# Kernel optimization log

Hardware: AMD Instinct MI355X
Metric: run time of the kernel (lower is better)

The kernel has to match this reference:

```python
import jax, jax.numpy as jnp
import numpy as np

S, T, I = 4096, 64, 64          # spatial cells, timesteps, input features
EH, E, H = 128, 256, 512        # embedding hidden, embedding size, LSTM hidden
LG, O, F1, F2 = 32, 128, 256, 64


def setup_inputs() -> dict:
    key = jax.random.key(0)
    ks = jax.random.split(key, 24)
    w = lambda k, shape: jax.random.normal(k, shape, jnp.float32) * 0.05
    return {
        "inputData": jax.random.normal(ks[0], (S, T, I), jnp.float32),
        "lane": jax.random.uniform(ks[1], (1, 1), jnp.float32),
        # lane gate MLP
        "Wlg1": w(ks[2], (LG, 1)),  "blg1": w(ks[3], (LG,)),
        "Wlg2": w(ks[4], (1, LG)),  "blg2": w(ks[5], (1,)),
        # embedding MLP
        "We1": w(ks[6], (EH, I)),   "be1": w(ks[7], (EH,)),
        "We2": w(ks[8], (E, EH)),   "be2": w(ks[9], (E,)),
        # LSTMCell params (torch layout: [4H, in]/[4H, H], gate order i,f,g,o)
        "Wih": w(ks[10], (4 * H, E)), "bih": w(ks[11], (4 * H,)),
        "Whh": w(ks[12], (4 * H, H)), "bhh": w(ks[13], (4 * H,)),
        # output head
        "Wout": w(ks[14], (O, H)),  "bout": w(ks[15], (O,)),
        "Wf1": w(ks[16], (F1, O)),  "bf1": w(ks[17], (F1,)),
        "Wf2": w(ks[18], (F2, F1)), "bf2": w(ks[19], (F2,)),
        "Wf3": w(ks[20], (1, F2)),  "bf3": w(ks[21], (1,)),
    }


def _spatial_maxpool(h):
    # MaxPool1d(kernel=3, stride=1, padding=1) over the spatial axis (axis 0),
    # implicit -inf padding as in torch maxpool.
    hp = jnp.pad(h, ((1, 1), (0, 0)), constant_values=-jnp.inf)
    return jnp.maximum(jnp.maximum(hp[:-2], hp[1:-1]), hp[2:])


def reference(inputData, lane, Wlg1, blg1, Wlg2, blg2, We1, be1, We2, be2,
              Wih, bih, Whh, bhh, Wout, bout, Wf1, bf1, Wf2, bf2, Wf3, bf3):
    # lane gate -> scalar in (0,1)
    lg = jax.nn.relu(lane @ Wlg1.T + blg1)
    laneC = jax.nn.sigmoid(lg @ Wlg2.T + blg2)          # [1,1]
    x = inputData * laneC.reshape(1, 1, 1)              # [S,T,I]
    # embedding MLP
    x = jax.nn.relu(x @ We1.T + be1)
    x = jax.nn.relu(x @ We2.T + be2)                    # [S,T,E]
    xt = jnp.transpose(x, (1, 0, 2))                    # [T,S,E]

    def step(carry, x_t):
        h, c = carry
        gates = x_t @ Wih.T + bih + h @ Whh.T + bhh     # [S,4H]
        i, f, g, o = jnp.split(gates, 4, axis=-1)
        c = jax.nn.sigmoid(f) * c + jax.nn.sigmoid(i) * jnp.tanh(g)
        h = jax.nn.sigmoid(o) * jnp.tanh(c)
        h = _spatial_maxpool(h)
        return (h, c), None

    h0 = jnp.zeros((inputData.shape[0], H), jnp.float32)
    c0 = jnp.zeros((inputData.shape[0], H), jnp.float32)
    (h, c), _ = jax.lax.scan(step, (h0, c0), xt)

    out = h @ Wout.T + bout
    out = jax.nn.relu(out @ Wf1.T + bf1)
    out = jax.nn.relu(out @ Wf2.T + bf2)
    out = out @ Wf3.T + bf3                             # [S,1]
    out = out / laneC.reshape(-1, 1)
    return (out, h, c)
```

## Files before the change

### kernel.cpp

```cpp
#include <hip/hip_runtime.h>
#include <hip/hip_bf16.h>
#include <cstdint>
#include <cstddef>

using bf16 = __hip_bfloat16;

typedef __attribute__((ext_vector_type(8))) short s8vec;
typedef __attribute__((ext_vector_type(4))) float f4vec;

#define SD 4096
#define TD 64
#define ID 64
#define EHD 128
#define ED 256
#define HD 512
#define GD 2048
#define OD 128
#define F1D 256
#define F2D 64

__device__ __forceinline__ float sigmf(float x) { return 1.0f / (1.0f + __expf(-x)); }
__device__ __forceinline__ float tanh_fast(float x) { return 1.0f - 2.0f / (__expf(2.0f * x) + 1.0f); }

__device__ __forceinline__ void async16(const bf16* g, void* lds) {
    __builtin_amdgcn_global_load_lds(
        (const __attribute__((address_space(1))) void*)g,
        (__attribute__((address_space(3))) void*)lds, 16, 0, 0);
}

__global__ __launch_bounds__(256, 4)
void lstm_gemm(const bf16* __restrict__ xt,
               const bf16* __restrict__ h,
               const bf16* __restrict__ Wpack,
               const float* __restrict__ biasg,
               const float* __restrict__ c_in,
               float* __restrict__ c_out,
               bf16* __restrict__ h_pre)
{
    __shared__ __align__(16) bf16 As[128 * 64];
    __shared__ __align__(16) bf16 Bs[64 * 64];

    const int tid = threadIdx.x;
    const int lane = tid & 63;
    const int wm = tid >> 6;
    const int m0 = blockIdx.x * 128, n0 = blockIdx.y * 64;
    const int lm = lane & 15, lq = lane >> 4;

    f4vec acc[2][4];
#pragma unroll
    for (int i = 0; i < 2; ++i)
#pragma unroll
        for (int j = 0; j < 4; ++j) acc[i][j] = (f4vec){0.f, 0.f, 0.f, 0.f};

    for (int kc = 0; kc < ED + HD; kc += 64) {
        const bf16* Ab; int Alda, kk;
        if (kc < ED) { Ab = xt; Alda = ED; kk = kc; }
        else         { Ab = h;  Alda = HD; kk = kc - ED; }

#pragma unroll
        for (int it = 0; it < 4; ++it) {
            int flat = it * 256 + tid;
            int row = flat >> 3, colu = flat & 7;
            const bf16* ga = Ab + (size_t)(m0 + row) * Alda + kk + colu * 8;
            uint32_t off = (uint32_t)(it * 256 + (tid & ~63)) * 16u;
            async16(ga, (char*)As + off);
        }
#pragma unroll
        for (int it = 0; it < 2; ++it) {
            int flat = it * 256 + tid;
            int row = flat >> 3, colu = flat & 7;
            const bf16* gb = Wpack + (size_t)(n0 + row) * (ED + HD) + kc + colu * 8;
            uint32_t off = (uint32_t)(it * 256 + (tid & ~63)) * 16u;
            async16(gb, (char*)Bs + off);
        }
        __syncthreads();

#pragma unroll
        for (int ks = 0; ks < 64; ks += 32) {
            s8vec af[2], bfr[4];
#pragma unroll
            for (int mi = 0; mi < 2; ++mi)
                af[mi] = *(const s8vec*)(As + (wm * 32 + mi * 16 + lm) * 64 + ks + lq * 8);
#pragma unroll
            for (int ni = 0; ni < 4; ++ni)
                bfr[ni] = *(const s8vec*)(Bs + (ni * 16 + lm) * 64 + ks + lq * 8);
#pragma unroll
            for (int mi = 0; mi < 2; ++mi)
#pragma unroll
                for (int ni = 0; ni < 4; ++ni)
                    acc[mi][ni] = __builtin_amdgcn_mfma_f32_16x16x32_bf16(af[mi], bfr[ni], acc[mi][ni], 0, 0, 0);
        }
        __syncthreads();
    }

    const int j = (n0 >> 2) + lm;
    const float bi = biasg[n0 + lm];
    const float bff = biasg[n0 + 16 + lm];
    const float bg = biasg[n0 + 32 + lm];
    const float bo = biasg[n0 + 48 + lm];
#pragma unroll
    for (int mi = 0; mi < 2; ++mi) {
#pragma unroll
        for (int r = 0; r < 4; ++r) {
            const int row = m0 + wm * 32 + mi * 16 + lq * 4 + r;
            float gi = acc[mi][0][r] + bi;
            float gf = acc[mi][1][r] + bff;
            float gg = acc[mi][2][r] + bg;
            float go = acc[mi][3][r] + bo;
            float cn = sigmf(gf) * c_in[(size_t)row * HD + j] + sigmf(gi) * tanh_fast(gg);
            c_out[(size_t)row * HD + j] = cn;
            h_pre[(size_t)row * HD + j] = __float2bfloat16(sigmf(go) * tanh_fast(cn));
        }
    }
}

constexpr int MODE_BF16 = 0;
constexpr int MODE_SCATTER = 2;

template <int MODE>
__global__ __launch_bounds__(256, 2)
void gemm_kernel(const bf16* __restrict__ A1, int lda1,
                 const bf16* __restrict__ B, int ldb,
                 const float* __restrict__ bias,
                 const float* __restrict__ scale,
                 int relu, void* __restrict__ Cp, int ldc,
                 int K, int ncols)
{
    __shared__ __align__(16) bf16 As[128 * 64];
    __shared__ __align__(16) bf16 Bs[128 * 64];

    const int tid = threadIdx.x;
    const int lane = tid & 63;
    const int w = tid >> 6;
    const int wm = w & 1, wn = w >> 1;
    const int m0 = blockIdx.x * 128, n0 = blockIdx.y * 128;
    const int lm = lane & 15, lq = lane >> 4;

    f4vec acc[4][4];
#pragma unroll
    for (int i = 0; i < 4; ++i)
#pragma unroll
        for (int j = 0; j < 4; ++j) acc[i][j] = (f4vec){0.f, 0.f, 0.f, 0.f};

    for (int kc = 0; kc < K; kc += 64) {
#pragma unroll
        for (int it = 0; it < 4; ++it) {
            int flat = it * 256 + tid;
            int row = flat >> 3, colu = flat & 7;
            const bf16* ga = A1 + (size_t)(m0 + row) * lda1 + kc + colu * 8;
            const bf16* gb = B + (size_t)(n0 + row) * ldb + kc + colu * 8;
            uint32_t off = (uint32_t)(it * 256 + (tid & ~63)) * 16u;
            async16(ga, (char*)As + off);
            async16(gb, (char*)Bs + off);
        }
        __syncthreads();

#pragma unroll
        for (int ks = 0; ks < 64; ks += 32) {
            s8vec af[4], bfr[4];
#pragma unroll
            for (int mi = 0; mi < 4; ++mi)
                af[mi] = *(const s8vec*)(As + (wm * 64 + mi * 16 + lm) * 64 + ks + lq * 8);
#pragma unroll
            for (int ni = 0; ni < 4; ++ni)
                bfr[ni] = *(const s8vec*)(Bs + (wn * 64 + ni * 16 + lm) * 64 + ks + lq * 8);
#pragma unroll
            for (int mi = 0; mi < 4; ++mi)
#pragma unroll
                for (int ni = 0; ni < 4; ++ni)
                    acc[mi][ni] = __builtin_amdgcn_mfma_f32_16x16x32_bf16(af[mi], bfr[ni], acc[mi][ni], 0, 0, 0);
        }
        __syncthreads();
    }

    const float sc = scale ? scale[0] : 1.0f;
#pragma unroll
    for (int mi = 0; mi < 4; ++mi) {
#pragma unroll
        for (int ni = 0; ni < 4; ++ni) {
            const int gcol = n0 + wn * 64 + ni * 16 + lm;
            const float bv = bias[gcol];
#pragma unroll
            for (int r = 0; r < 4; ++r) {
                const int grow = m0 + wm * 64 + mi * 16 + lq * 4 + r;
                float v = acc[mi][ni][r] * sc + bv;
                if (relu) v = fmaxf(v, 0.f);
                if constexpr (MODE == MODE_BF16) {
                    if (gcol < ncols)
                        ((bf16*)Cp)[(size_t)grow * ldc + gcol] = __float2bfloat16(v);
                } else {
                    const int crow = (grow & 63) * SD + (grow >> 6);
                    ((bf16*)Cp)[(size_t)crow * ldc + gcol] = __float2bfloat16(v);
                }
            }
        }
    }
}

__global__ void prep_kernel(const float* __restrict__ Wih, const float* __restrict__ Whh,
                            const float* __restrict__ bih, const float* __restrict__ bhh,
                            const float* __restrict__ We1, const float* __restrict__ We2,
                            const float* __restrict__ Wout, const float* __restrict__ Wf1,
                            const float* __restrict__ Wf2, const float* __restrict__ bf2,
                            bf16* __restrict__ Wpack, float* __restrict__ biasg,
                            bf16* __restrict__ We1b, bf16* __restrict__ We2b,
                            bf16* __restrict__ Woutb, bf16* __restrict__ Wf1b,
                            bf16* __restrict__ Wf2p, float* __restrict__ bf2f)
{
    int idx = blockIdx.x * 256 + threadIdx.x;
    const int S0 = GD * (ED + HD);
    if (idx < S0) {
        int p = idx / (ED + HD), k = idx - p * (ED + HD);
        int gate = (p >> 4) & 3;
        int j = (p >> 6) * 16 + (p & 15);
        int orig = gate * HD + j;
        float v = (k < ED) ? Wih[(size_t)orig * ED + k] : Whh[(size_t)orig * HD + (k - ED)];
        Wpack[idx] = __float2bfloat16(v);
        return;
    }
    idx -= S0;
    if (idx < GD) {
        int p = idx;
        int gate = (p >> 4) & 3;
        int j = (p >> 6) * 16 + (p & 15);
        int orig = gate * HD + j;
        biasg[p] = bih[orig] + bhh[orig];
        return;
    }
    idx -= GD;
    if (idx < EHD * ID) { We1b[idx] = __float2bfloat16(We1[idx]); return; }
    idx -= EHD * ID;
    if (idx < ED * EHD) { We2b[idx] = __float2bfloat16(We2[idx]); return; }
    idx -= ED * EHD;
    if (idx < OD * HD) { Woutb[idx] = __float2bfloat16(Wout[idx]); return; }
    idx -= OD * HD;
    if (idx < F1D * OD) { Wf1b[idx] = __float2bfloat16(Wf1[idx]); return; }
    idx -= F1D * OD;
    if (idx < 128 * F1D) {
        int nrow = idx >> 8;
        Wf2p[idx] = (nrow < F2D) ? __float2bfloat16(Wf2[idx]) : __float2bfloat16(0.f);
        return;
    }
    idx -= 128 * F1D;
    if (idx < 128) { bf2f[idx] = (idx < F2D) ? bf2[idx] : 0.f; return; }
}

__global__ void cvt_input_kernel(const float* __restrict__ src, bf16* __restrict__ dst)
{
    int i = (blockIdx.x * 256 + threadIdx.x) * 8;
    float4 a = *(const float4*)(src + i);
    float4 b = *(const float4*)(src + i + 4);
    bf16 o[8] = { __float2bfloat16(a.x), __float2bfloat16(a.y),
                  __float2bfloat16(a.z), __float2bfloat16(a.w),
                  __float2bfloat16(b.x), __float2bfloat16(b.y),
                  __float2bfloat16(b.z), __float2bfloat16(b.w) };
    *(uint4*)(dst + i) = *(const uint4*)o;
}

__global__ void lane_kernel(const float* __restrict__ lane, const float* __restrict__ Wlg1,
                            const float* __restrict__ blg1, const float* __restrict__ Wlg2,
                            const float* __restrict__ blg2, float* __restrict__ laneC)
{
    if (threadIdx.x != 0) return;
    const float l = lane[0];
    float acc = blg2[0];
    for (int k = 0; k < 32; ++k)
        acc += fmaxf(l * Wlg1[k] + blg1[k], 0.f) * Wlg2[k];
    float v = 1.f / (1.f + __expf(-acc));
    laneC[0] = v;
    laneC[1] = 1.f / v;
}

__global__ void zero_kernel(float* __restrict__ c0, bf16* __restrict__ h)
{
    int idx = blockIdx.x * 256 + threadIdx.x;
    if (idx < SD * HD) { c0[idx] = 0.f; h[idx] = __float2bfloat16(0.f); }
}

__global__ void maxpool_kernel(const bf16* __restrict__ hp, bf16* __restrict__ hout)
{
    int base = (blockIdx.x * 256 + threadIdx.x) * 8;
    int s = base >> 9;
    const uint4 vm = *(const uint4*)(hp + base);
    const unsigned short* m = (const unsigned short*)&vm;
    uint4 vu, vd;
    const unsigned short* u = nullptr; const unsigned short* d = nullptr;
    if (s > 0)      { vu = *(const uint4*)(hp + base - HD); u = (const unsigned short*)&vu; }
    if (s < SD - 1) { vd = *(const uint4*)(hp + base + HD); d = (const unsigned short*)&vd; }
    unsigned short o[8];
#pragma unroll
    for (int e = 0; e < 8; ++e) {
        float v = __bfloat162float(__ushort_as_bfloat16(m[e]));
        if (u) v = fmaxf(v, __bfloat162float(__ushort_as_bfloat16(u[e])));
        if (d) v = fmaxf(v, __bfloat162float(__ushort_as_bfloat16(d[e])));
        o[e] = __bfloat16_as_ushort(__float2bfloat16(v));
    }
    *(uint4*)(hout + base) = *(const uint4*)o;
}

__global__ void f3_kernel(const bf16* __restrict__ xf2, const float* __restrict__ Wf3,
                          const float* __restrict__ bf3, const float* __restrict__ laneC,
                          float* __restrict__ out)
{
    int s = blockIdx.x * 256 + threadIdx.x;
    if (s >= SD) return;
    float acc = bf3[0];
#pragma unroll
    for (int k = 0; k < F2D; ++k)
        acc += __bfloat162float(xf2[(size_t)s * F2D + k]) * Wf3[k];
    out[s] = acc * laneC[1];
}

__global__ void finalize_kernel(const bf16* __restrict__ h, const float* __restrict__ c,
                                float* __restrict__ out)
{
    int idx = (blockIdx.x * 256 + threadIdx.x) * 4;
    if (idx >= SD * HD) return;
    uint2 hv4 = *(const uint2*)(h + idx);
    const unsigned short* hu = (const unsigned short*)&hv4;
    float4 hf = { __bfloat162float(__ushort_as_bfloat16(hu[0])),
                  __bfloat162float(__ushort_as_bfloat16(hu[1])),
                  __bfloat162float(__ushort_as_bfloat16(hu[2])),
                  __bfloat162float(__ushort_as_bfloat16(hu[3])) };
    *(float4*)(out + SD + idx) = hf;
    *(float4*)(out + SD + SD * HD + idx) = *(const float4*)(c + idx);
}

extern "C" void kernel_launch(void* const* d_in, const int* in_sizes, int n_in,
                              void* d_out, int out_size, void* d_ws, size_t ws_size,
                              hipStream_t stream)
{
    (void)in_sizes; (void)n_in; (void)out_size;
    const float* inputDataF = (const float*)d_in[0];
    const float* lane = (const float*)d_in[1];
    const float* Wlg1 = (const float*)d_in[2];
    const float* blg1 = (const float*)d_in[3];
    const float* Wlg2 = (const float*)d_in[4];
    const float* blg2 = (const float*)d_in[5];
    const float* We1 = (const float*)d_in[6];
    const float* be1 = (const float*)d_in[7];
    const float* We2 = (const float*)d_in[8];
    const float* be2 = (const float*)d_in[9];
    const float* Wih = (const float*)d_in[10];
    const float* bih = (const float*)d_in[11];
    const float* Whh = (const float*)d_in[12];
    const float* bhh = (const float*)d_in[13];
    const float* Wout = (const float*)d_in[14];
    const float* bout = (const float*)d_in[15];
    const float* Wf1 = (const float*)d_in[16];
    const float* bf1 = (const float*)d_in[17];
    const float* Wf2 = (const float*)d_in[18];
    const float* bf2 = (const float*)d_in[19];
    const float* Wf3 = (const float*)d_in[20];
    const float* bf3 = (const float*)d_in[21];
    float* out = (float*)d_out;

    char* wp = (char*)d_ws;
    auto carve = [&](size_t bytes) { char* p = wp; wp += (bytes + 255) & ~(size_t)255; return p; };

    bf16* inb   = (bf16*)carve((size_t)SD * TD * ID * 2);
    float* laneCbuf = (float*)carve(2 * sizeof(float));
    float* cbuf0 = (float*)carve((size_t)SD * HD * 4);
    float* cbuf1 = (float*)carve((size_t)SD * HD * 4);
    bf16* hbuf  = (bf16*)carve((size_t)SD * HD * 2);
    bf16* hpre  = (bf16*)carve((size_t)SD * HD * 2);
    bf16* Wpack = (bf16*)carve((size_t)GD * (ED + HD) * 2);
    float* biasg = (float*)carve(GD * 4);
    float* bf2f = (float*)carve(128 * 4);
    bf16* We1b  = (bf16*)carve((size_t)EHD * ID * 2);
    bf16* We2b  = (bf16*)carve((size_t)ED * EHD * 2);
    bf16* Woutb = (bf16*)carve((size_t)OD * HD * 2);
    bf16* Wf1b  = (bf16*)carve((size_t)F1D * OD * 2);
    bf16* Wf2p  = (bf16*)carve((size_t)128 * F1D * 2);
    bf16* out_o = (bf16*)carve((size_t)SD * OD * 2);
    bf16* xf1   = (bf16*)carve((size_t)SD * F1D * 2);
    bf16* xf2   = (bf16*)carve((size_t)SD * F2D * 2);

    const size_t SZ_X1 = (size_t)SD * TD * EHD * 2;
    const size_t SZ_X2 = (size_t)SD * TD * ED * 2;
    const size_t used = (size_t)(wp - (char*)d_ws);
    const size_t remain = (ws_size > used) ? (ws_size - used) : 0;
    const bool persist = remain >= (SZ_X1 + SZ_X2 + 4096);

    bf16* x1 = nullptr; bf16* x2 = nullptr;
    bf16* x1t = nullptr; bf16* x2t = nullptr;
    if (persist) {
        x1 = (bf16*)carve(SZ_X1);
        x2 = (bf16*)carve(SZ_X2);
    } else {
        x1t = (bf16*)carve((size_t)SD * EHD * 2);
        x2t = (bf16*)carve((size_t)SD * ED * 2);
    }

    const int PREP_N = GD * (ED + HD) + GD + EHD * ID + ED * EHD + OD * HD
                     + F1D * OD + 128 * F1D + 128;

    cvt_input_kernel<<<SD * TD * ID / (256 * 8), 256, 0, stream>>>(inputDataF, inb);
    prep_kernel<<<(PREP_N + 255) / 256, 256, 0, stream>>>(
        Wih, Whh, bih, bhh, We1, We2, Wout, Wf1, Wf2, bf2,
        Wpack, biasg, We1b, We2b, Woutb, Wf1b, Wf2p, bf2f);
    lane_kernel<<<1, 64, 0, stream>>>(lane, Wlg1, blg1, Wlg2, blg2, laneCbuf);
    zero_kernel<<<SD * HD / 256, 256, 0, stream>>>(cbuf0, hbuf);

    if (persist) {
        gemm_kernel<MODE_BF16><<<dim3(SD * TD / 128, 1), 256, 0, stream>>>(
            inb, ID, We1b, ID, be1, laneCbuf, 1, x1, EHD, ID, EHD);
        gemm_kernel<MODE_SCATTER><<<dim3(SD * TD / 128, ED / 128), 256, 0, stream>>>(
            x1, EHD, We2b, EHD, be2, nullptr, 1, x2, ED, EHD, ED);
    }

    for (int t = 0; t < TD; ++t) {
        const float* c_in = (t & 1) ? cbuf1 : cbuf0;
        float* c_out = (t & 1) ? cbuf0 : cbuf1;
        const bf16* xA;
        if (persist) {
            xA = x2 + (size_t)t * SD * ED;
        } else {
            gemm_kernel<MODE_BF16><<<dim3(SD / 128, 1), 256, 0, stream>>>(
                inb + (size_t)t * ID, TD * ID, We1b, ID, be1, laneCbuf, 1,
                x1t, EHD, ID, EHD);
            gemm_kernel<MODE_BF16><<<dim3(SD / 128, ED / 128), 256, 0, stream>>>(
                x1t, EHD, We2b, EHD, be2, nullptr, 1, x2t, ED, EHD, ED);
            xA = x2t;
        }
        lstm_gemm<<<dim3(SD / 128, GD / 64), 256, 0, stream>>>(
            xA, hbuf, Wpack, biasg, c_in, c_out, hpre);
        maxpool_kernel<<<SD * HD / (256 * 8), 256, 0, stream>>>(hpre, hbuf);
    }

    gemm_kernel<MODE_BF16><<<dim3(SD / 128, 1), 256, 0, stream>>>(
        hbuf, HD, Woutb, HD, bout, nullptr, 0, out_o, OD, HD, OD);
    gemm_kernel<MODE_BF16><<<dim3(SD / 128, F1D / 128), 256, 0, stream>>>(
        out_o, OD, Wf1b, OD, bf1, nullptr, 1, xf1, F1D, OD, F1D);
    gemm_kernel<MODE_BF16><<<dim3(SD / 128, 1), 256, 0, stream>>>(
        xf1, F1D, Wf2p, F1D, bf2f, nullptr, 1, xf2, F2D, F1D, F2D);
    f3_kernel<<<SD / 256, 256, 0, stream>>>(xf2, Wf3, bf3, laneCbuf, out);
    finalize_kernel<<<SD * HD / (256 * 4), 256, 0, stream>>>(hbuf, cbuf0, out);
}
```

Baseline: 2.466 ms.

## Run LSTM recurrence as persistent cooperative kernel with register-resident cell state

Replaces the 64 per-timestep lstm_gemm and maxpool launch pairs with one cooperative kernel that loops over timesteps and synchronises the grid between steps. The cell state stays in registers across steps, and the spatial maxpool is folded into the h-tile load. Tiles widen to 128x128 with a new weight/bias packing to match. The aim is to cut launch overhead and the round trips of c and h_pre through memory, at the cost of grid-wide barriers, a 256-block grid that must be co-resident, and synchronous (non-async) loads for the fused maxpool.

```diff
diff --git a/kernel.cpp b/kernel.cpp
--- a/kernel.cpp
+++ b/kernel.cpp
@@ -1,8 +1,10 @@
 #include <hip/hip_runtime.h>
 #include <hip/hip_bf16.h>
+#include <hip/hip_cooperative_groups.h>
 #include <cstdint>
 #include <cstddef>
 
+namespace cg = cooperative_groups;
 using bf16 = __hip_bfloat16;
 
 typedef __attribute__((ext_vector_type(8))) short s8vec;
@@ -28,64 +30,187 @@
         (__attribute__((address_space(3))) void*)lds, 16, 0, 0);
 }
 
-__global__ __launch_bounds__(256, 4)
-void lstm_gemm(const bf16* __restrict__ xt,
-               const bf16* __restrict__ h,
-               const bf16* __restrict__ Wpack,
-               const float* __restrict__ biasg,
-               const float* __restrict__ c_in,
-               float* __restrict__ c_out,
-               bf16* __restrict__ h_pre)
-{
+__device__ __forceinline__ float bfbits2f(unsigned short u) {
+    union { unsigned int i; float f; } v; v.i = (unsigned int)u << 16; return v.f;
+}
+
+__device__ __forceinline__ uint4 bfmax8(uint4 a, uint4 b) {
+    const unsigned short* pa = (const unsigned short*)&a;
+    const unsigned short* pb = (const unsigned short*)&b;
+    uint4 r; unsigned short* pr = (unsigned short*)&r;
+#pragma unroll
+    for (int e = 0; e < 8; ++e)
+        pr[e] = (bfbits2f(pa[e]) > bfbits2f(pb[e])) ? pa[e] : pb[e];
+    return r;
+}
+
+__global__ __launch_bounds__(256, 2)
+void lstm_persistent(const bf16* __restrict__ x2,
+                     bf16* __restrict__ hpA,
+                     bf16* __restrict__ hpB,
+                     const bf16* __restrict__ Wpack,
+                     const float* __restrict__ biasg,
+                     float* __restrict__ cbuf)
+{
+    cg::grid_group grid = cg::this_grid();
     __shared__ __align__(16) bf16 As[128 * 64];
-    __shared__ __align__(16) bf16 Bs[64 * 64];
+    __shared__ __align__(16) bf16 Bs[128 * 64];
 
     const int tid = threadIdx.x;
     const int lane = tid & 63;
-    const int wm = tid >> 6;
-    const int m0 = blockIdx.x * 128, n0 = blockIdx.y * 64;
+    const int w = tid >> 6;
+    const int wm = w & 1, wn = w >> 1;
+    const int m0 = blockIdx.x * 128, n0 = blockIdx.y * 128;
     const int lm = lane & 15, lq = lane >> 4;
-
-    f4vec acc[2][4];
-#pragma unroll
-    for (int i = 0; i < 2; ++i)
-#pragma unroll
-        for (int j = 0; j < 4; ++j) acc[i][j] = (f4vec){0.f, 0.f, 0.f, 0.f};
+    const int j = (n0 >> 2) + wn * 16 + lm;
+    const float bi = biasg[n0 + wn * 64 + lm];
+    const float bff = biasg[n0 + wn * 64 + 16 + lm];
+    const float bg = biasg[n0 + wn * 64 + 32 + lm];
+    const float bo = biasg[n0 + wn * 64 + 48 + lm];
+
+    float c_reg[4][4];
+#pragma unroll
+    for (int mi = 0; mi < 4; ++mi)
+#pragma unroll
+        for (int r = 0; r < 4; ++r) c_reg[mi][r] = 0.f;
+
+    for (int t = 0; t < TD; ++t) {
+        const bf16* xt = x2 + (size_t)t * SD * ED;
+        const bf16* hR = (t & 1) ? hpA : hpB;
+        bf16* hW = (t & 1) ? hpB : hpA;
+
+        f4vec acc[4][4];
+#pragma unroll
+        for (int i = 0; i < 4; ++i)
+#pragma unroll
+            for (int jj = 0; jj < 4; ++jj) acc[i][jj] = (f4vec){0.f, 0.f, 0.f, 0.f};
+
+        for (int kc = 0; kc < ED + HD; kc += 64) {
+            if (kc < ED) {
+#pragma unroll
+                for (int it = 0; it < 4; ++it) {
+                    int flat = it * 256 + tid;
+                    int row = flat >> 3, colu = flat & 7;
+                    const bf16* ga = xt + (size_t)(m0 + row) * ED + kc + colu * 8;
+                    uint32_t off = (uint32_t)(it * 256 + (tid & ~63)) * 16u;
+                    async16(ga, (char*)As + off);
+                }
+            } else {
+                const int kk = kc - ED;
+#pragma unroll
+                for (int it = 0; it < 4; ++it) {
+                    int flat = it * 256 + tid;
+                    int row = flat >> 3, colu = flat & 7;
+                    int s = m0 + row;
+                    const bf16* base = hR + (size_t)s * HD + kk + colu * 8;
+                    uint4 res = *(const uint4*)base;
+                    if (s > 0)      res = bfmax8(res, *(const uint4*)(base - HD));
+                    if (s < SD - 1) res = bfmax8(res, *(const uint4*)(base + HD));
+                    *(uint4*)(As + flat * 8) = res;
+                }
+            }
+#pragma unroll
+            for (int it = 0; it < 4; ++it) {
+                int flat = it * 256 + tid;
+                int row = flat >> 3, colu = flat & 7;
+                const bf16* gb = Wpack + (size_t)(n0 + row) * (ED + HD) + kc + colu * 8;
+                uint32_t off = (uint32_t)(it * 256 + (tid & ~63)) * 16u;
+                async16(gb, (char*)Bs + off);
+            }
+            __syncthreads();
+#pragma unroll
+            for (int ks = 0; ks < 64; ks += 32) {
+                s8vec af[4], bfr[4];
+#pragma unroll
+                for (int mi = 0; mi < 4; ++mi)
+                    af[mi] = *(const s8vec*)(As + (wm * 64 + mi * 16 + lm) * 64 + ks + lq * 8);
+#pragma unroll
+                for (int ni = 0; ni < 4; ++ni)
+                    bfr[ni] = *(const s8vec*)(Bs + (wn * 64 + ni * 16 + lm) * 64 + ks + lq * 8);
+#pragma unroll
+                for (int mi = 0; mi < 4; ++mi)
+#pragma unroll
+                    for (int ni = 0; ni < 4; ++ni)
+                        acc[mi][ni] = __builtin_amdgcn_mfma_f32_16x16x32_bf16(af[mi], bfr[ni], acc[mi][ni], 0, 0, 0);
+            }
+            __syncthreads();
+        }
+
+#pragma unroll
+        for (int mi = 0; mi < 4; ++mi) {
+#pragma unroll
+            for (int r = 0; r < 4; ++r) {
+                const int row = m0 + wm * 64 + mi * 16 + lq * 4 + r;
+                float gi = acc[mi][0][r] + bi;
+                float gf = acc[mi][1][r] + bff;
+                float gg = acc[mi][2][r] + bg;
+                float go = acc[mi][3][r] + bo;
+                float cn = sigmf(gf) * c_reg[mi][r] + sigmf(gi) * tanh_fast(gg);
+                c_reg[mi][r] = cn;
+                hW[(size_t)row * HD + j] = __float2bfloat16(sigmf(go) * tanh_fast(cn));
+            }
+        }
+        __threadfence();
+        grid.sync();
+    }
+
+#pragma unroll
+    for (int mi = 0; mi < 4; ++mi)
+#pragma unroll
+        for (int r = 0; r < 4; ++r) {
+            const int row = m0 + wm * 64 + mi * 16 + lq * 4 + r;
+            cbuf[(size_t)row * HD + j] = c_reg[mi][r];
+        }
+}
+
+__global__ __launch_bounds__(256, 2)
+void lstm_step(const bf16* __restrict__ xt, const bf16* __restrict__ hbuf,
+               const bf16* __restrict__ Wpack, const float* __restrict__ biasg,
+               const float* __restrict__ c_in, float* __restrict__ c_out,
+               bf16* __restrict__ h_pre)
+{
+    __shared__ __align__(16) bf16 As[128 * 64];
+    __shared__ __align__(16) bf16 Bs[128 * 64];
+
+    const int tid = threadIdx.x;
+    const int lane = tid & 63;
+    const int w = tid >> 6;
+    const int wm = w & 1, wn = w >> 1;
+    const int m0 = blockIdx.x * 128, n0 = blockIdx.y * 128;
+    const int lm = lane & 15, lq = lane >> 4;
+
+    f4vec acc[4][4];
+#pragma unroll
+    for (int i = 0; i < 4; ++i)
+#pragma unroll
+        for (int jj = 0; jj < 4; ++jj) acc[i][jj] = (f4vec){0.f, 0.f, 0.f, 0.f};
 
     for (int kc = 0; kc < ED + HD; kc += 64) {
         const bf16* Ab; int Alda, kk;
-        if (kc < ED) { Ab = xt; Alda = ED; kk = kc; }
-        else         { Ab = h;  Alda = HD; kk = kc - ED; }
-
+        if (kc < ED) { Ab = xt;   Alda = ED; kk = kc; }
+        else         { Ab = hbuf; Alda = HD; kk = kc - ED; }
 #pragma unroll
         for (int it = 0; it < 4; ++it) {
             int flat = it * 256 + tid;
             int row = flat >> 3, colu = flat & 7;
             const bf16* ga = Ab + (size_t)(m0 + row) * Alda + kk + colu * 8;
+            const bf16* gb = Wpack + (size_t)(n0 + row) * (ED + HD) + kc + colu * 8;
             uint32_t off = (uint32_t)(it * 256 + (tid & ~63)) * 16u;
             async16(ga, (char*)As + off);
-        }
-#pragma unroll
-        for (int it = 0; it < 2; ++it) {
-            int flat = it * 256 + tid;
-            int row = flat >> 3, colu = flat & 7;
-            const bf16* gb = Wpack + (size_t)(n0 + row) * (ED + HD) + kc + colu * 8;
-            uint32_t off = (uint32_t)(it * 256 + (tid & ~63)) * 16u;
             async16(gb, (char*)Bs + off);
         }
         __syncthreads();
-
 #pragma unroll
         for (int ks = 0; ks < 64; ks += 32) {
-            s8vec af[2], bfr[4];
-#pragma unroll
-            for (int mi = 0; mi < 2; ++mi)
-                af[mi] = *(const s8vec*)(As + (wm * 32 + mi * 16 + lm) * 64 + ks + lq * 8);
+            s8vec af[4], bfr[4];
+#pragma unroll
+            for (int mi = 0; mi < 4; ++mi)
+                af[mi] = *(const s8vec*)(As + (wm * 64 + mi * 16 + lm) * 64 + ks + lq * 8);
 #pragma unroll
             for (int ni = 0; ni < 4; ++ni)
-                bfr[ni] = *(const s8vec*)(Bs + (ni * 16 + lm) * 64 + ks + lq * 8);
-#pragma unroll
-            for (int mi = 0; mi < 2; ++mi)
+                bfr[ni] = *(const s8vec*)(Bs + (wn * 64 + ni * 16 + lm) * 64 + ks + lq * 8);
+#pragma unroll
+            for (int mi = 0; mi < 4; ++mi)
 #pragma unroll
                 for (int ni = 0; ni < 4; ++ni)
                     acc[mi][ni] = __builtin_amdgcn_mfma_f32_16x16x32_bf16(af[mi], bfr[ni], acc[mi][ni], 0, 0, 0);
@@ -93,16 +218,16 @@
         __syncthreads();
     }
 
-    const int j = (n0 >> 2) + lm;
-    const float bi = biasg[n0 + lm];
-    const float bff = biasg[n0 + 16 + lm];
-    const float bg = biasg[n0 + 32 + lm];
-    const float bo = biasg[n0 + 48 + lm];
-#pragma unroll
-    for (int mi = 0; mi < 2; ++mi) {
+    const int j = (n0 >> 2) + wn * 16 + lm;
+    const float bi = biasg[n0 + wn * 64 + lm];
+    const float bff = biasg[n0 + wn * 64 + 16 + lm];
+    const float bg = biasg[n0 + wn * 64 + 32 + lm];
+    const float bo = biasg[n0 + wn * 64 + 48 + lm];
+#pragma unroll
+    for (int mi = 0; mi < 4; ++mi) {
 #pragma unroll
         for (int r = 0; r < 4; ++r) {
-            const int row = m0 + wm * 32 + mi * 16 + lq * 4 + r;
+            const int row = m0 + wm * 64 + mi * 16 + lq * 4 + r;
             float gi = acc[mi][0][r] + bi;
             float gf = acc[mi][1][r] + bff;
             float gg = acc[mi][2][r] + bg;
@@ -140,7 +265,7 @@
 #pragma unroll
     for (int i = 0; i < 4; ++i)
 #pragma unroll
-        for (int j = 0; j < 4; ++j) acc[i][j] = (f4vec){0.f, 0.f, 0.f, 0.f};
+        for (int jj = 0; jj < 4; ++jj) acc[i][jj] = (f4vec){0.f, 0.f, 0.f, 0.f};
 
     for (int kc = 0; kc < K; kc += 64) {
 #pragma unroll
@@ -154,7 +279,6 @@
             async16(gb, (char*)Bs + off);
         }
         __syncthreads();
-
 #pragma unroll
         for (int ks = 0; ks < 64; ks += 32) {
             s8vec af[4], bfr[4];
@@ -211,19 +335,20 @@
     const int S0 = GD * (ED + HD);
     if (idx < S0) {
         int p = idx / (ED + HD), k = idx - p * (ED + HD);
-        int gate = (p >> 4) & 3;
-        int j = (p >> 6) * 16 + (p & 15);
-        int orig = gate * HD + j;
+        int q = p & 127;
+        int jv = (p >> 7) * 32 + ((q >> 6) << 4) + (q & 15);
+        int gate = (q >> 4) & 3;
+        int orig = gate * HD + jv;
         float v = (k < ED) ? Wih[(size_t)orig * ED + k] : Whh[(size_t)orig * HD + (k - ED)];
         Wpack[idx] = __float2bfloat16(v);
         return;
     }
     idx -= S0;
     if (idx < GD) {
-        int p = idx;
-        int gate = (p >> 4) & 3;
-        int j = (p >> 6) * 16 + (p & 15);
-        int orig = gate * HD + j;
+        int p = idx, q = p & 127;
+        int jv = (p >> 7) * 32 + ((q >> 6) << 4) + (q & 15);
+        int gate = (q >> 4) & 3;
+        int orig = gate * HD + jv;
         biasg[p] = bih[orig] + bhh[orig];
         return;
     }
@@ -271,31 +396,25 @@
     laneC[1] = 1.f / v;
 }
 
-__global__ void zero_kernel(float* __restrict__ c0, bf16* __restrict__ h)
+__global__ void zero_kernel(float* __restrict__ c0, bf16* __restrict__ h,
+                            bf16* __restrict__ hp)
 {
     int idx = blockIdx.x * 256 + threadIdx.x;
-    if (idx < SD * HD) { c0[idx] = 0.f; h[idx] = __float2bfloat16(0.f); }
+    if (idx < SD * HD) {
+        c0[idx] = 0.f;
+        h[idx] = __float2bfloat16(0.f);
+        hp[idx] = __float2bfloat16(0.f);
+    }
 }
 
 __global__ void maxpool_kernel(const bf16* __restrict__ hp, bf16* __restrict__ hout)
 {
     int base = (blockIdx.x * 256 + threadIdx.x) * 8;
     int s = base >> 9;
-    const uint4 vm = *(const uint4*)(hp + base);
-    const unsigned short* m = (const unsigned short*)&vm;
-    uint4 vu, vd;
-    const unsigned short* u = nullptr; const unsigned short* d = nullptr;
-    if (s > 0)      { vu = *(const uint4*)(hp + base - HD); u = (const unsigned short*)&vu; }
-    if (s < SD - 1) { vd = *(const uint4*)(hp + base + HD); d = (const unsigned short*)&vd; }
-    unsigned short o[8];
-#pragma unroll
-    for (int e = 0; e < 8; ++e) {
-        float v = __bfloat162float(__ushort_as_bfloat16(m[e]));
-        if (u) v = fmaxf(v, __bfloat162float(__ushort_as_bfloat16(u[e])));
-        if (d) v = fmaxf(v, __bfloat162float(__ushort_as_bfloat16(d[e])));
-        o[e] = __bfloat16_as_ushort(__float2bfloat16(v));
-    }
-    *(uint4*)(hout + base) = *(const uint4*)o;
+    uint4 res = *(const uint4*)(hp + base);
+    if (s > 0)      res = bfmax8(res, *(const uint4*)(hp + base - HD));
+    if (s < SD - 1) res = bfmax8(res, *(const uint4*)(hp + base + HD));
+    *(uint4*)(hout + base) = res;
 }
 
 __global__ void f3_kernel(const bf16* __restrict__ xf2, const float* __restrict__ Wf3,
@@ -318,10 +437,7 @@
     if (idx >= SD * HD) return;
     uint2 hv4 = *(const uint2*)(h + idx);
     const unsigned short* hu = (const unsigned short*)&hv4;
-    float4 hf = { __bfloat162float(__ushort_as_bfloat16(hu[0])),
-                  __bfloat162float(__ushort_as_bfloat16(hu[1])),
-                  __bfloat162float(__ushort_as_bfloat16(hu[2])),
-                  __bfloat162float(__ushort_as_bfloat16(hu[3])) };
+    float4 hf = { bfbits2f(hu[0]), bfbits2f(hu[1]), bfbits2f(hu[2]), bfbits2f(hu[3]) };
     *(float4*)(out + SD + idx) = hf;
     *(float4*)(out + SD + SD * HD + idx) = *(const float4*)(c + idx);
 }
@@ -363,7 +479,8 @@
     float* cbuf0 = (float*)carve((size_t)SD * HD * 4);
     float* cbuf1 = (float*)carve((size_t)SD * HD * 4);
     bf16* hbuf  = (bf16*)carve((size_t)SD * HD * 2);
-    bf16* hpre  = (bf16*)carve((size_t)SD * HD * 2);
+    bf16* hpA   = (bf16*)carve((size_t)SD * HD * 2);
+    bf16* hpB   = (bf16*)carve((size_t)SD * HD * 2);
     bf16* Wpack = (bf16*)carve((size_t)GD * (ED + HD) * 2);
     float* biasg = (float*)carve(GD * 4);
     float* bf2f = (float*)carve(128 * 4);
@@ -400,32 +517,45 @@
         Wih, Whh, bih, bhh, We1, We2, Wout, Wf1, Wf2, bf2,
         Wpack, biasg, We1b, We2b, Woutb, Wf1b, Wf2p, bf2f);
     lane_kernel<<<1, 64, 0, stream>>>(lane, Wlg1, blg1, Wlg2, blg2, laneCbuf);
-    zero_kernel<<<SD * HD / 256, 256, 0, stream>>>(cbuf0, hbuf);
-
+    zero_kernel<<<SD * HD / 256, 256, 0, stream>>>(cbuf0, hbuf, hpB);
+
+    bool coop_ok = false;
     if (persist) {
         gemm_kernel<MODE_BF16><<<dim3(SD * TD / 128, 1), 256, 0, stream>>>(
             inb, ID, We1b, ID, be1, laneCbuf, 1, x1, EHD, ID, EHD);
         gemm_kernel<MODE_SCATTER><<<dim3(SD * TD / 128, ED / 128), 256, 0, stream>>>(
             x1, EHD, We2b, EHD, be2, nullptr, 1, x2, ED, EHD, ED);
-    }
-
-    for (int t = 0; t < TD; ++t) {
-        const float* c_in = (t & 1) ? cbuf1 : cbuf0;
-        float* c_out = (t & 1) ? cbuf0 : cbuf1;
-        const bf16* xA;
-        if (persist) {
-            xA = x2 + (size_t)t * SD * ED;
-        } else {
-            gemm_kernel<MODE_BF16><<<dim3(SD / 128, 1), 256, 0, stream>>>(
-                inb + (size_t)t * ID, TD * ID, We1b, ID, be1, laneCbuf, 1,
-                x1t, EHD, ID, EHD);
-            gemm_kernel<MODE_BF16><<<dim3(SD / 128, ED / 128), 256, 0, stream>>>(
-                x1t, EHD, We2b, EHD, be2, nullptr, 1, x2t, ED, EHD, ED);
-            xA = x2t;
-        }
-        lstm_gemm<<<dim3(SD / 128, GD / 64), 256, 0, stream>>>(
-            xA, hbuf, Wpack, biasg, c_in, c_out, hpre);
-        maxpool_kernel<<<SD * HD / (256 * 8), 256, 0, stream>>>(hpre, hbuf);
+
+        void* args[] = { (void*)&x2, (void*)&hpA, (void*)&hpB,
+                         (void*)&Wpack, (void*)&biasg, (void*)&cbuf0 };
+        hipError_t cerr = hipLaunchCooperativeKernel(
+            (const void*)lstm_persistent, dim3(SD / 128, GD / 128), dim3(256),
+            args, 0, stream);
+        if (cerr == hipSuccess) {
+            coop_ok = true;
+            maxpool_kernel<<<SD * HD / (256 * 8), 256, 0, stream>>>(hpB, hbuf);
+        }
+    }
+
+    if (!coop_ok) {
+        for (int t = 0; t < TD; ++t) {
+            const float* c_in = (t & 1) ? cbuf1 : cbuf0;
+            float* c_out = (t & 1) ? cbuf0 : cbuf1;
+            const bf16* xA;
+            if (persist) {
+                xA = x2 + (size_t)t * SD * ED;
+            } else {
+                gemm_kernel<MODE_BF16><<<dim3(SD / 128, 1), 256, 0, stream>>>(
+                    inb + (size_t)t * ID, TD * ID, We1b, ID, be1, laneCbuf, 1,
+                    x1t, EHD, ID, EHD);
+                gemm_kernel<MODE_BF16><<<dim3(SD / 128, ED / 128), 256, 0, stream>>>(
+                    x1t, EHD, We2b, EHD, be2, nullptr, 1, x2t, ED, EHD, ED);
+                xA = x2t;
+            }
+            lstm_step<<<dim3(SD / 128, GD / 128), 256, 0, stream>>>(
+                xA, hbuf, Wpack, biasg, c_in, c_out, hpA);
+            maxpool_kernel<<<SD * HD / (256 * 8), 256, 0, stream>>>(hpA, hbuf);
+        }
     }
 
     gemm_kernel<MODE_BF16><<<dim3(SD / 128, 1), 256, 0, stream>>>(
```

After: 2.991 ms. 1.21x slower.

## Fuse spatial maxpool into LSTM GEMM and pre-swizzle operands into MFMA fragment layout

Applied to the files above, without the earlier changes.

The per-step maxpool kernel is removed. Each LSTM step now reads the previous pre-pool h, applies the 3-neighbour max while staging the A tile into LDS, and writes a ping-ponged pre-pool h, with a single maxpool run after the loop. The x and weight operands are pre-packed into MFMA fragment order so they can be bulk-copied with contiguous async loads, and the tile grows to 128x128 with a K chunk of 128. This drops a launch and an extra read/write of h per step. In exchange, the h loads become synchronous register loads with three row reads each, and LDS use and register pressure increase.

```diff
diff --git a/kernel.cpp b/kernel.cpp
--- a/kernel.cpp
+++ b/kernel.cpp
@@ -28,64 +28,96 @@
         (__attribute__((address_space(3))) void*)lds, 16, 0, 0);
 }
 
-__global__ __launch_bounds__(256, 4)
-void lstm_gemm(const bf16* __restrict__ xt,
-               const bf16* __restrict__ h,
-               const bf16* __restrict__ Wpack,
-               const float* __restrict__ biasg,
-               const float* __restrict__ c_in,
-               float* __restrict__ c_out,
-               bf16* __restrict__ h_pre)
-{
-    __shared__ __align__(16) bf16 As[128 * 64];
-    __shared__ __align__(16) bf16 Bs[64 * 64];
+__device__ __forceinline__ float bfbits2f(unsigned short u) {
+    union { unsigned int i; float f; } v; v.i = (unsigned int)u << 16; return v.f;
+}
+
+__device__ __forceinline__ uint4 bfmax8(uint4 a, uint4 b) {
+    const unsigned short* pa = (const unsigned short*)&a;
+    const unsigned short* pb = (const unsigned short*)&b;
+    uint4 r; unsigned short* pr = (unsigned short*)&r;
+#pragma unroll
+    for (int e = 0; e < 8; ++e)
+        pr[e] = (bfbits2f(pa[e]) > bfbits2f(pb[e])) ? pa[e] : pb[e];
+    return r;
+}
+
+__device__ __forceinline__ int frag_off(int row, int k) {
+    int wq = row >> 6, mi = (row >> 4) & 3, lm = row & 15;
+    int ks = (k >> 5) & 3, lq = (k >> 3) & 3, e8 = k & 7;
+    return ((((wq * 4 + ks) * 4 + mi) * 64 + lq * 16 + lm) << 3) + e8;
+}
+
+__global__ __launch_bounds__(256, 2)
+void lstm_fused(const bf16* __restrict__ xF,
+                const bf16* __restrict__ hR,
+                bf16* __restrict__ hW,
+                const bf16* __restrict__ WpackF,
+                const float* __restrict__ biasg,
+                const float* __restrict__ c_in,
+                float* __restrict__ c_out)
+{
+    __shared__ __align__(16) bf16 As[128 * 128];
+    __shared__ __align__(16) bf16 Bs[128 * 128];
 
     const int tid = threadIdx.x;
     const int lane = tid & 63;
-    const int wm = tid >> 6;
-    const int m0 = blockIdx.x * 128, n0 = blockIdx.y * 64;
+    const int w = tid >> 6;
+    const int wm = w & 1, wn = w >> 1;
+    const int mt = blockIdx.x, nt = blockIdx.y;
+    const int m0 = mt * 128, n0 = nt * 128;
     const int lm = lane & 15, lq = lane >> 4;
 
-    f4vec acc[2][4];
-#pragma unroll
-    for (int i = 0; i < 2; ++i)
-#pragma unroll
-        for (int j = 0; j < 4; ++j) acc[i][j] = (f4vec){0.f, 0.f, 0.f, 0.f};
-
-    for (int kc = 0; kc < ED + HD; kc += 64) {
-        const bf16* Ab; int Alda, kk;
-        if (kc < ED) { Ab = xt; Alda = ED; kk = kc; }
-        else         { Ab = h;  Alda = HD; kk = kc - ED; }
-
-#pragma unroll
-        for (int it = 0; it < 4; ++it) {
-            int flat = it * 256 + tid;
-            int row = flat >> 3, colu = flat & 7;
-            const bf16* ga = Ab + (size_t)(m0 + row) * Alda + kk + colu * 8;
-            uint32_t off = (uint32_t)(it * 256 + (tid & ~63)) * 16u;
-            async16(ga, (char*)As + off);
-        }
-#pragma unroll
-        for (int it = 0; it < 2; ++it) {
-            int flat = it * 256 + tid;
-            int row = flat >> 3, colu = flat & 7;
-            const bf16* gb = Wpack + (size_t)(n0 + row) * (ED + HD) + kc + colu * 8;
-            uint32_t off = (uint32_t)(it * 256 + (tid & ~63)) * 16u;
-            async16(gb, (char*)Bs + off);
+    f4vec acc[4][4];
+#pragma unroll
+    for (int i = 0; i < 4; ++i)
+#pragma unroll
+        for (int jj = 0; jj < 4; ++jj) acc[i][jj] = (f4vec){0.f, 0.f, 0.f, 0.f};
+
+    for (int ki = 0; ki < 6; ++ki) {
+        if (ki < 2) {
+            const bf16* src = xF + ((size_t)(mt * 2 + ki) << 14);
+#pragma unroll
+            for (int it = 0; it < 8; ++it) {
+                uint32_t off = (uint32_t)(it * 256 + (tid & ~63)) * 16u;
+                async16(src + (size_t)(it * 256 + tid) * 8, (char*)As + off);
+            }
+        } else {
+            const int kkj = (ki - 2) * 128;
+#pragma unroll
+            for (int it = 0; it < 8; ++it) {
+                int s = it * 256 + tid;
+                int sl = s & 63;
+                int mi = (s >> 6) & 3, ks = (s >> 8) & 3, wq = s >> 10;
+                int row = m0 + wq * 64 + mi * 16 + (sl & 15);
+                int jj = kkj + ks * 32 + (sl >> 4) * 8;
+                const bf16* base = hR + (size_t)row * HD + jj;
+                uint4 v = *(const uint4*)base;
+                if (row > 0)      v = bfmax8(v, *(const uint4*)(base - HD));
+                if (row < SD - 1) v = bfmax8(v, *(const uint4*)(base + HD));
+                *(uint4*)(As + s * 8) = v;
+            }
+        }
+        {
+            const bf16* src = WpackF + ((size_t)(nt * 6 + ki) << 14);
+#pragma unroll
+            for (int it = 0; it < 8; ++it) {
+                uint32_t off = (uint32_t)(it * 256 + (tid & ~63)) * 16u;
+                async16(src + (size_t)(it * 256 + tid) * 8, (char*)Bs + off);
+            }
         }
         __syncthreads();
-
-#pragma unroll
-        for (int ks = 0; ks < 64; ks += 32) {
-            s8vec af[2], bfr[4];
-#pragma unroll
-            for (int mi = 0; mi < 2; ++mi)
-                af[mi] = *(const s8vec*)(As + (wm * 32 + mi * 16 + lm) * 64 + ks + lq * 8);
+#pragma unroll
+        for (int ks = 0; ks < 4; ++ks) {
+            s8vec af[4], bfr[4];
+#pragma unroll
+            for (int mi = 0; mi < 4; ++mi)
+                af[mi] = *(const s8vec*)(As + ((wm * 4 + ks) * 4 + mi) * 512 + lane * 8);
 #pragma unroll
             for (int ni = 0; ni < 4; ++ni)
-                bfr[ni] = *(const s8vec*)(Bs + (ni * 16 + lm) * 64 + ks + lq * 8);
-#pragma unroll
-            for (int mi = 0; mi < 2; ++mi)
+                bfr[ni] = *(const s8vec*)(Bs + ((wn * 4 + ks) * 4 + ni) * 512 + lane * 8);
+#pragma unroll
+            for (int mi = 0; mi < 4; ++mi)
 #pragma unroll
                 for (int ni = 0; ni < 4; ++ni)
                     acc[mi][ni] = __builtin_amdgcn_mfma_f32_16x16x32_bf16(af[mi], bfr[ni], acc[mi][ni], 0, 0, 0);
@@ -93,29 +125,30 @@
         __syncthreads();
     }
 
-    const int j = (n0 >> 2) + lm;
-    const float bi = biasg[n0 + lm];
-    const float bff = biasg[n0 + 16 + lm];
-    const float bg = biasg[n0 + 32 + lm];
-    const float bo = biasg[n0 + 48 + lm];
-#pragma unroll
-    for (int mi = 0; mi < 2; ++mi) {
+    const int j = (n0 >> 2) + wn * 16 + lm;
+    const float bi = biasg[n0 + wn * 64 + lm];
+    const float bff = biasg[n0 + wn * 64 + 16 + lm];
+    const float bg = biasg[n0 + wn * 64 + 32 + lm];
+    const float bo = biasg[n0 + wn * 64 + 48 + lm];
+#pragma unroll
+    for (int mi = 0; mi < 4; ++mi) {
 #pragma unroll
         for (int r = 0; r < 4; ++r) {
-            const int row = m0 + wm * 32 + mi * 16 + lq * 4 + r;
+            const int row = m0 + wm * 64 + mi * 16 + lq * 4 + r;
             float gi = acc[mi][0][r] + bi;
             float gf = acc[mi][1][r] + bff;
             float gg = acc[mi][2][r] + bg;
             float go = acc[mi][3][r] + bo;
             float cn = sigmf(gf) * c_in[(size_t)row * HD + j] + sigmf(gi) * tanh_fast(gg);
             c_out[(size_t)row * HD + j] = cn;
-            h_pre[(size_t)row * HD + j] = __float2bfloat16(sigmf(go) * tanh_fast(cn));
+            hW[(size_t)row * HD + j] = __float2bfloat16(sigmf(go) * tanh_fast(cn));
         }
     }
 }
 
 constexpr int MODE_BF16 = 0;
 constexpr int MODE_SCATTER = 2;
+constexpr int MODE_FRAG = 3;
 
 template <int MODE>
 __global__ __launch_bounds__(256, 2)
@@ -140,7 +173,7 @@
 #pragma unroll
     for (int i = 0; i < 4; ++i)
 #pragma unroll
-        for (int j = 0; j < 4; ++j) acc[i][j] = (f4vec){0.f, 0.f, 0.f, 0.f};
+        for (int jj = 0; jj < 4; ++jj) acc[i][jj] = (f4vec){0.f, 0.f, 0.f, 0.f};
 
     for (int kc = 0; kc < K; kc += 64) {
 #pragma unroll
@@ -154,7 +187,6 @@
             async16(gb, (char*)Bs + off);
         }
         __syncthreads();
-
 #pragma unroll
         for (int ks = 0; ks < 64; ks += 32) {
             s8vec af[4], bfr[4];
@@ -188,9 +220,16 @@
                 if constexpr (MODE == MODE_BF16) {
                     if (gcol < ncols)
                         ((bf16*)Cp)[(size_t)grow * ldc + gcol] = __float2bfloat16(v);
+                } else if constexpr (MODE == MODE_SCATTER) {
+                    int t = grow & 63, s = grow >> 6;
+                    size_t addr = (size_t)t * (SD * ED)
+                                + (size_t)((((s >> 7) * 2 + (gcol >> 7)) << 14)
+                                           + frag_off(s & 127, gcol & 127));
+                    ((bf16*)Cp)[addr] = __float2bfloat16(v);
                 } else {
-                    const int crow = (grow & 63) * SD + (grow >> 6);
-                    ((bf16*)Cp)[(size_t)crow * ldc + gcol] = __float2bfloat16(v);
+                    size_t addr = (size_t)((((grow >> 7) * 2 + (gcol >> 7)) << 14)
+                                           + frag_off(grow & 127, gcol & 127));
+                    ((bf16*)Cp)[addr] = __float2bfloat16(v);
                 }
             }
         }
@@ -202,7 +241,7 @@
                             const float* __restrict__ We1, const float* __restrict__ We2,
                             const float* __restrict__ Wout, const float* __restrict__ Wf1,
                             const float* __restrict__ Wf2, const float* __restrict__ bf2,
-                            bf16* __restrict__ Wpack, float* __restrict__ biasg,
+                            bf16* __restrict__ WpackF, float* __restrict__ biasg,
                             bf16* __restrict__ We1b, bf16* __restrict__ We2b,
                             bf16* __restrict__ Woutb, bf16* __restrict__ Wf1b,
                             bf16* __restrict__ Wf2p, float* __restrict__ bf2f)
@@ -210,20 +249,26 @@
     int idx = blockIdx.x * 256 + threadIdx.x;
     const int S0 = GD * (ED + HD);
     if (idx < S0) {
-        int p = idx / (ED + HD), k = idx - p * (ED + HD);
-        int gate = (p >> 4) & 3;
-        int j = (p >> 6) * 16 + (p & 15);
-        int orig = gate * HD + j;
-        float v = (k < ED) ? Wih[(size_t)orig * ED + k] : Whh[(size_t)orig * HD + (k - ED)];
-        Wpack[idx] = __float2bfloat16(v);
+        int tile = idx >> 14;
+        int within = idx & 16383;
+        int slot = within >> 3, e8 = within & 7;
+        int nt = tile / 6, ki = tile - nt * 6;
+        int lanev = slot & 63, lmv = lanev & 15, lqv = lanev >> 4;
+        int ni = (slot >> 6) & 3, ks = (slot >> 8) & 3, wnv = slot >> 10;
+        int j = nt * 32 + wnv * 16 + lmv;
+        int orig = ni * HD + j;
+        int kg = ki * 128 + ks * 32 + lqv * 8 + e8;
+        float v = (kg < ED) ? Wih[(size_t)orig * ED + kg]
+                            : Whh[(size_t)orig * HD + (kg - ED)];
+        WpackF[idx] = __float2bfloat16(v);
         return;
     }
     idx -= S0;
     if (idx < GD) {
-        int p = idx;
-        int gate = (p >> 4) & 3;
-        int j = (p >> 6) * 16 + (p & 15);
-        int orig = gate * HD + j;
+        int p = idx, q = p & 127;
+        int jv = (p >> 7) * 32 + ((q >> 6) << 4) + (q & 15);
+        int gate = (q >> 4) & 3;
+        int orig = gate * HD + jv;
         biasg[p] = bih[orig] + bhh[orig];
         return;
     }
@@ -271,31 +316,23 @@
     laneC[1] = 1.f / v;
 }
 
-__global__ void zero_kernel(float* __restrict__ c0, bf16* __restrict__ h)
+__global__ void zero_kernel(float* __restrict__ c0, bf16* __restrict__ hp)
 {
     int idx = blockIdx.x * 256 + threadIdx.x;
-    if (idx < SD * HD) { c0[idx] = 0.f; h[idx] = __float2bfloat16(0.f); }
+    if (idx < SD * HD) {
+        c0[idx] = 0.f;
+        hp[idx] = __float2bfloat16(0.f);
+    }
 }
 
 __global__ void maxpool_kernel(const bf16* __restrict__ hp, bf16* __restrict__ hout)
 {
     int base = (blockIdx.x * 256 + threadIdx.x) * 8;
     int s = base >> 9;
-    const uint4 vm = *(const uint4*)(hp + base);
-    const unsigned short* m = (const unsigned short*)&vm;
-    uint4 vu, vd;
-    const unsigned short* u = nullptr; const unsigned short* d = nullptr;
-    if (s > 0)      { vu = *(const uint4*)(hp + base - HD); u = (const unsigned short*)&vu; }
-    if (s < SD - 1) { vd = *(const uint4*)(hp + base + HD); d = (const unsigned short*)&vd; }
-    unsigned short o[8];
-#pragma unroll
-    for (int e = 0; e < 8; ++e) {
-        float v = __bfloat162float(__ushort_as_bfloat16(m[e]));
-        if (u) v = fmaxf(v, __bfloat162float(__ushort_as_bfloat16(u[e])));
-        if (d) v = fmaxf(v, __bfloat162float(__ushort_as_bfloat16(d[e])));
-        o[e] = __bfloat16_as_ushort(__float2bfloat16(v));
-    }
-    *(uint4*)(hout + base) = *(const uint4*)o;
+    uint4 res = *(const uint4*)(hp + base);
+    if (s > 0)      res = bfmax8(res, *(const uint4*)(hp + base - HD));
+    if (s < SD - 1) res = bfmax8(res, *(const uint4*)(hp + base + HD));
+    *(uint4*)(hout + base) = res;
 }
 
 __global__ void f3_kernel(const bf16* __restrict__ xf2, const float* __restrict__ Wf3,
@@ -318,10 +355,7 @@
     if (idx >= SD * HD) return;
     uint2 hv4 = *(const uint2*)(h + idx);
     const unsigned short* hu = (const unsigned short*)&hv4;
-    float4 hf = { __bfloat162float(__ushort_as_bfloat16(hu[0])),
-                  __bfloat162float(__ushort_as_bfloat16(hu[1])),
-                  __bfloat162float(__ushort_as_bfloat16(hu[2])),
-                  __bfloat162float(__ushort_as_bfloat16(hu[3])) };
+    float4 hf = { bfbits2f(hu[0]), bfbits2f(hu[1]), bfbits2f(hu[2]), bfbits2f(hu[3]) };
     *(float4*)(out + SD + idx) = hf;
     *(float4*)(out + SD + SD * HD + idx) = *(const float4*)(c + idx);
 }
@@ -363,8 +397,9 @@
     float* cbuf0 = (float*)carve((size_t)SD * HD * 4);
     float* cbuf1 = (float*)carve((size_t)SD * HD * 4);
     bf16* hbuf  = (bf16*)carve((size_t)SD * HD * 2);
-    bf16* hpre  = (bf16*)carve((size_t)SD * HD * 2);
-    bf16* Wpack = (bf16*)carve((size_t)GD * (ED + HD) * 2);
+    bf16* hpA   = (bf16*)carve((size_t)SD * HD * 2);
+    bf16* hpB   = (bf16*)carve((size_t)SD * HD * 2);
+    bf16* WpackF = (bf16*)carve((size_t)GD * (ED + HD) * 2);
     float* biasg = (float*)carve(GD * 4);
     float* bf2f = (float*)carve(128 * 4);
     bf16* We1b  = (bf16*)carve((size_t)EHD * ID * 2);
@@ -382,14 +417,14 @@
     const size_t remain = (ws_size > used) ? (ws_size - used) : 0;
     const bool persist = remain >= (SZ_X1 + SZ_X2 + 4096);
 
-    bf16* x1 = nullptr; bf16* x2 = nullptr;
-    bf16* x1t = nullptr; bf16* x2t = nullptr;
+    bf16* x1 = nullptr; bf16* x2F = nullptr;
+    bf16* x1t = nullptr; bf16* x2tF = nullptr;
     if (persist) {
         x1 = (bf16*)carve(SZ_X1);
-        x2 = (bf16*)carve(SZ_X2);
+        x2F = (bf16*)carve(SZ_X2);
     } else {
         x1t = (bf16*)carve((size_t)SD * EHD * 2);
-        x2t = (bf16*)carve((size_t)SD * ED * 2);
+        x2tF = (bf16*)carve((size_t)SD * ED * 2);
     }
 
     const int PREP_N = GD * (ED + HD) + GD + EHD * ID + ED * EHD + OD * HD
@@ -398,35 +433,37 @@
     cvt_input_kernel<<<SD * TD * ID / (256 * 8), 256, 0, stream>>>(inputDataF, inb);
     prep_kernel<<<(PREP_N + 255) / 256, 256, 0, stream>>>(
         Wih, Whh, bih, bhh, We1, We2, Wout, Wf1, Wf2, bf2,
-        Wpack, biasg, We1b, We2b, Woutb, Wf1b, Wf2p, bf2f);
+        WpackF, biasg, We1b, We2b, Woutb, Wf1b, Wf2p, bf2f);
     lane_kernel<<<1, 64, 0, stream>>>(lane, Wlg1, blg1, Wlg2, blg2, laneCbuf);
-    zero_kernel<<<SD * HD / 256, 256, 0, stream>>>(cbuf0, hbuf);
+    zero_kernel<<<SD * HD / 256, 256, 0, stream>>>(cbuf0, hpB);
 
     if (persist) {
         gemm_kernel<MODE_BF16><<<dim3(SD * TD / 128, 1), 256, 0, stream>>>(
             inb, ID, We1b, ID, be1, laneCbuf, 1, x1, EHD, ID, EHD);
         gemm_kernel<MODE_SCATTER><<<dim3(SD * TD / 128, ED / 128), 256, 0, stream>>>(
-            x1, EHD, We2b, EHD, be2, nullptr, 1, x2, ED, EHD, ED);
+            x1, EHD, We2b, EHD, be2, nullptr, 1, x2F, ED, EHD, ED);
     }
 
     for (int t = 0; t < TD; ++t) {
         const float* c_in = (t & 1) ? cbuf1 : cbuf0;
         float* c_out = (t & 1) ? cbuf0 : cbuf1;
-        const bf16* xA;
+        const bf16* hR = (t & 1) ? hpA : hpB;
+        bf16* hW = (t & 1) ? hpB : hpA;
+        const bf16* xF;
         if (persist) {
-            xA = x2 + (size_t)t * SD * ED;
+            xF = x2F + (size_t)t * SD * ED;
         } else {
             gemm_kernel<MODE_BF16><<<dim3(SD / 128, 1), 256, 0, stream>>>(
                 inb + (size_t)t * ID, TD * ID, We1b, ID, be1, laneCbuf, 1,
                 x1t, EHD, ID, EHD);
-            gemm_kernel<MODE_BF16><<<dim3(SD / 128, ED / 128), 256, 0, stream>>>(
-                x1t, EHD, We2b, EHD, be2, nullptr, 1, x2t, ED, EHD, ED);
-            xA = x2t;
-        }
-        lstm_gemm<<<dim3(SD / 128, GD / 64), 256, 0, stream>>>(
-            xA, hbuf, Wpack, biasg, c_in, c_out, hpre);
-        maxpool_kernel<<<SD * HD / (256 * 8), 256, 0, stream>>>(hpre, hbuf);
-    }
+            gemm_kernel<MODE_FRAG><<<dim3(SD / 128, ED / 128), 256, 0, stream>>>(
+                x1t, EHD, We2b, EHD, be2, nullptr, 1, x2tF, ED, EHD, ED);
+            xF = x2tF;
+        }
+        lstm_fused<<<dim3(SD / 128, GD / 128), 256, 0, stream>>>(
+            xF, hR, hW, WpackF, biasg, c_in, c_out);
+    }
+    maxpool_kernel<<<SD * HD / (256 * 8), 256, 0, stream>>>(hpB, hbuf);
 
     gemm_kernel<MODE_BF16><<<dim3(SD / 128, 1), 256, 0, stream>>>(
         hbuf, HD, Woutb, HD, bout, nullptr, 0, out_o, OD, HD, OD);
```

Result: slower. 3.468 ms (+40.6%).
